# Kernel tuning notes

Measured on AMD Instinct MI355X. Metric: run time of the kernel, lower is better.

The kernel has to match this reference:

```python
import jax, jax.numpy as jnp
import numpy as np

B, T, D, H = 256, 512, 512, 512


def setup_inputs() -> dict:
    key = jax.random.key(0)
    k0, k1, k2, k3 = jax.random.split(key, 4)
    sD = 1.0 / np.sqrt(D).astype(np.float32)
    sH = 1.0 / np.sqrt(H).astype(np.float32)
    return {
        "x": jax.random.normal(k0, (B, T, D), jnp.float32),
        "Wx": jax.random.normal(k1, (D, 4 * H), jnp.float32) * sD,
        "Wh": jax.random.normal(k2, (H, 4 * H), jnp.float32) * sH,
        "b": jnp.zeros((4 * H,), jnp.float32),
        "Wfc": jax.random.normal(k3, (H, 1), jnp.float32) * sH,
        "bfc": jnp.zeros((1,), jnp.float32),
    }


def reference(x, Wx, Wh, b, Wfc, bfc):
    # x: [B, T, D]. Flax LSTMCell gates (i, f, g, o):
    #   i,f,o = sigmoid(.), g = tanh(.); c' = f*c + i*g; h' = o*tanh(c')
    Bv, Tv, _ = x.shape
    Hv = Wh.shape[0]
    # Precompute all input projections in one big GEMM (same math, batched).
    xg = jnp.einsum('btd,dg->btg', x, Wx) + b  # [B, T, 4H]

    def step(carry, xt):
        c, h = carry
        gates = xt + h @ Wh                     # [B, 4H]
        i, f, g, o = jnp.split(gates, 4, axis=-1)
        c_new = jax.nn.sigmoid(f) * c + jax.nn.sigmoid(i) * jnp.tanh(g)
        h_new = jax.nn.sigmoid(o) * jnp.tanh(c_new)
        return (c_new, h_new), None

    c0 = jnp.zeros((Bv, Hv), x.dtype)
    h0 = jnp.zeros((Bv, Hv), x.dtype)
    (c_fin, h_fin), _ = jax.lax.scan(step, (c0, h0), jnp.swapaxes(xg, 0, 1))
    # fc applied to last timestep output (== final hidden state)
    return h_fin @ Wfc + bfc  # [B, 1]
```

## Files before the change

kernel.cpp:

```cpp
#include <hip/hip_runtime.h>
#include <hip/hip_bf16.h>


typedef _Float16 half8 __attribute__((ext_vector_type(8)));
typedef _Float16 half4 __attribute__((ext_vector_type(4)));
typedef int int4v __attribute__((ext_vector_type(4)));
typedef float float4v __attribute__((ext_vector_type(4)));

__device__ __forceinline__ void gl_lds16(const void* g, void* l) {
  __builtin_amdgcn_global_load_lds(
      (const __attribute__((address_space(1))) unsigned int*)g,
      (__attribute__((address_space(3))) unsigned int*)l, 16, 0, 0);
}

__device__ __forceinline__ float sigm(float v) { return 1.f / (1.f + __expf(-v)); }
__device__ __forceinline__ float tanh_(float v) { return 1.f - 2.f / (__expf(2.f * v) + 1.f); }

__global__ __launch_bounds__(256) void k_prep(
    const float* __restrict__ x, const float* __restrict__ Wx,
    const float* __restrict__ Wh, const float* __restrict__ b,
    _Float16* __restrict__ xf, _Float16* __restrict__ wxt,
    _Float16* __restrict__ wht, float* __restrict__ bp)
{
  const long NX8 = 67108864L / 8;
  const long NW  = 2048L * 512;
  const long TOT = NX8 + 2 * NW + 2048;
  long stride = (long)gridDim.x * blockDim.x;
  for (long id = (long)blockIdx.x * blockDim.x + threadIdx.x; id < TOT; id += stride) {
    if (id < NX8) {
      const float4v* p = (const float4v*)x + id * 2;
      float4v a = p[0], c = p[1];
      half8 o;
      o[0]=(_Float16)a[0]; o[1]=(_Float16)a[1]; o[2]=(_Float16)a[2]; o[3]=(_Float16)a[3];
      o[4]=(_Float16)c[0]; o[5]=(_Float16)c[1]; o[6]=(_Float16)c[2]; o[7]=(_Float16)c[3];
      ((half8*)xf)[id] = o;
    } else if (id < NX8 + NW) {
      long e = id - NX8;
      int np = (int)(e >> 9), k = (int)(e & 511);
      int j = np >> 2, gt = np & 3;
      wxt[e] = (_Float16)Wx[(long)k * 2048 + gt * 512 + j];
    } else if (id < NX8 + 2 * NW) {
      long e = id - NX8 - NW;
      int np = (int)(e >> 9), k = (int)(e & 511);
      int j = np >> 2, gt = np & 3;
      wht[e] = (_Float16)Wh[(long)k * 2048 + gt * 512 + j];
    } else {
      int np = (int)(id - NX8 - 2 * NW);
      int j = np >> 2, gt = np & 3;
      bp[np] = b[gt * 512 + j];
    }
  }
}

__global__ __launch_bounds__(256, 2) void k_gemm_xg(
    const _Float16* __restrict__ xf, const _Float16* __restrict__ wxt,
    const float* __restrict__ bp, _Float16* __restrict__ xg)
{
  __shared__ _Float16 As[128 * 32];
  __shared__ _Float16 Bs[128 * 32];
  const int tid = threadIdx.x;
  const int w = tid >> 6, l = tid & 63;
  const int mt = blockIdx.x >> 4, nt = blockIdx.x & 15;
  const int qr = (w >> 1) * 64, qc = (w & 1) * 64;
  float4v acc[4][4];
  #pragma unroll
  for (int i = 0; i < 4; ++i)
    #pragma unroll
    for (int j = 0; j < 4; ++j) acc[i][j] = (float4v){0.f, 0.f, 0.f, 0.f};
  const int lr = l >> 2, lc = (l & 3) * 8;
  for (int kt = 0; kt < 16; ++kt) {
    __syncthreads();
    #pragma unroll
    for (int i = 0; i < 2; ++i) {
      int chunk = i * 4 + w;
      gl_lds16(xf + ((long)(mt * 128 + chunk * 16 + lr)) * 512 + kt * 32 + lc, As + chunk * 512);
      gl_lds16(wxt + ((long)(nt * 128 + chunk * 16 + lr)) * 512 + kt * 32 + lc, Bs + chunk * 512);
    }
    __syncthreads();
    half8 af[4], bf[4];
    #pragma unroll
    for (int mi = 0; mi < 4; ++mi)
      af[mi] = *(const half8*)(As + (qr + mi * 16 + (l & 15)) * 32 + (l >> 4) * 8);
    #pragma unroll
    for (int ni = 0; ni < 4; ++ni)
      bf[ni] = *(const half8*)(Bs + (qc + ni * 16 + (l & 15)) * 32 + (l >> 4) * 8);
    #pragma unroll
    for (int mi = 0; mi < 4; ++mi)
      #pragma unroll
      for (int ni = 0; ni < 4; ++ni)
        acc[mi][ni] = __builtin_amdgcn_mfma_f32_16x16x32_f16(af[mi], bf[ni], acc[mi][ni], 0, 0, 0);
  }
  #pragma unroll
  for (int ni = 0; ni < 4; ++ni) {
    int col = nt * 128 + qc + ni * 16 + (l & 15);
    float bias = bp[col];
    #pragma unroll
    for (int mi = 0; mi < 4; ++mi) {
      long R0 = (long)mt * 128 + qr + mi * 16 + (l >> 4) * 4;
      #pragma unroll
      for (int r = 0; r < 4; ++r)
        xg[(R0 + r) * 2048 + col] = (_Float16)(acc[mi][ni][r] + bias);
    }
  }
}

__global__ __launch_bounds__(256, 1) void k_scan(
    const _Float16* __restrict__ xg, const _Float16* __restrict__ wht,
    const float* __restrict__ wfc, const float* __restrict__ bfc,
    _Float16* __restrict__ hsl, unsigned int* __restrict__ flags,
    float* __restrict__ out)
{
  __shared__ unsigned int wctr;
  const int tid = threadIdx.x;
  if (tid == 0) wctr = 0;
  __syncthreads();

  const int w = tid >> 6, l = tid & 63;
  const int q = l >> 4;
  const int m = l & 15;
  const int bb = blockIdx.x;
  const int slot = bb >> 3;
  const int g = (bb & 7) * 2 + (slot >> 4);
  const int s = slot & 15;

  int4v bw0[16], bw1[16];
  {
    const _Float16* b0 = wht + ((long)(s * 128 + (2 * w + 0) * 16 + m)) * 512 + q * 8;
    const _Float16* b1 = wht + ((long)(s * 128 + (2 * w + 1) * 16 + m)) * 512 + q * 8;
    #pragma unroll
    for (int kk = 0; kk < 16; ++kk) {
      bw0[kk] = *(const int4v*)(b0 + kk * 32);
      bw1[kk] = *(const int4v*)(b1 + kk * 32);
    }
    #pragma unroll
    for (int kk = 0; kk < 16; ++kk)
      asm volatile("" : "+v"(bw0[kk]), "+v"(bw1[kk]));
  }

  float c0 = 0.f, c1 = 0.f;
  const int j0 = s * 32 + 8 * w + q;
  const int j1 = s * 32 + 8 * w + 4 + q;
  const float wf0 = wfc[j0], wf1 = wfc[j1];
  unsigned int* fl = flags + g * 256;
  const _Float16* xgr = xg + ((long)(g * 16 + m)) * 512 * 2048 + s * 128 + q * 4;
  const _Float16* hrg = hsl + (long)g * 8192 + q * 128 + m * 8;
  _Float16* hw = hsl + (long)(g * 16 + s) * 512 + w * 128 + m * 8;

  half4 xc0 = *(const half4*)(xgr + (2 * w + 0) * 16);
  half4 xc1 = *(const half4*)(xgr + (2 * w + 1) * 16);

  for (int t = 0; t < 512; ++t) {
    const int pr = t & 1;
    const long tn = (t < 511) ? (long)(t + 1) : 511L;
    const half4 xn0 = *(const half4*)(xgr + tn * 2048 + (2 * w + 0) * 16);
    const half4 xn1 = *(const half4*)(xgr + tn * 2048 + (2 * w + 1) * 16);
    if (t) {
      if (w == 0 && l < 16 && l != s) {
        unsigned int* p = fl + l * 16;
        while (__hip_atomic_load(p, __ATOMIC_RELAXED, __HIP_MEMORY_SCOPE_AGENT)
               < (unsigned)t) {}
      }
      asm volatile("" ::: "memory");
      __syncthreads();
    }
    const _Float16* hr = hrg + pr * 131072;
    int4v av[16];
    #pragma unroll
    for (int kk = 0; kk < 16; ++kk)
      asm volatile("global_load_dwordx4 %0, %1, off sc0 sc1"
                   : "=&v"(av[kk]) : "v"(hr + kk * 512) : "memory");
    asm volatile("s_waitcnt vmcnt(0)" ::: "memory");
    __builtin_amdgcn_sched_barrier(0);

    float4v a0 = (float4v){0.f,0.f,0.f,0.f}, a1 = a0, b0v = a0, b1v = a0;
    #pragma unroll
    for (int kk = 0; kk < 8; ++kk) {
      a0 = __builtin_amdgcn_mfma_f32_16x16x32_f16(__builtin_bit_cast(half8, bw0[kk]),
                                                  __builtin_bit_cast(half8, av[kk]), a0, 0, 0, 0);
      a1 = __builtin_amdgcn_mfma_f32_16x16x32_f16(__builtin_bit_cast(half8, bw1[kk]),
                                                  __builtin_bit_cast(half8, av[kk]), a1, 0, 0, 0);
    }
    #pragma unroll
    for (int kk = 8; kk < 16; ++kk) {
      b0v = __builtin_amdgcn_mfma_f32_16x16x32_f16(__builtin_bit_cast(half8, bw0[kk]),
                                                   __builtin_bit_cast(half8, av[kk]), b0v, 0, 0, 0);
      b1v = __builtin_amdgcn_mfma_f32_16x16x32_f16(__builtin_bit_cast(half8, bw1[kk]),
                                                   __builtin_bit_cast(half8, av[kk]), b1v, 0, 0, 0);
    }
    a0 += b0v; a1 += b1v;
    float i0 = sigm(a0[0] + (float)xc0[0]);
    float f0 = sigm(a0[1] + (float)xc0[1]);
    float g0 = tanh_(a0[2] + (float)xc0[2]);
    float o0 = sigm(a0[3] + (float)xc0[3]);
    c0 = f0 * c0 + i0 * g0;
    float h0v = o0 * tanh_(c0);
    float i1 = sigm(a1[0] + (float)xc1[0]);
    float f1 = sigm(a1[1] + (float)xc1[1]);
    float g1 = tanh_(a1[2] + (float)xc1[2]);
    float o1 = sigm(a1[3] + (float)xc1[3]);
    c1 = f1 * c1 + i1 * g1;
    float h1v = o1 * tanh_(c1);
    unsigned int hb0 = (unsigned int)__builtin_bit_cast(unsigned short, (_Float16)h0v);
    unsigned int hb1 = (unsigned int)__builtin_bit_cast(unsigned short, (_Float16)h1v);
    unsigned int pb0 = __shfl_xor(hb0, 16);
    unsigned int pb1 = __shfl_xor(hb1, 16);
    unsigned int pair0 = hb0 | (pb0 << 16);
    unsigned int pair1 = hb1 | (pb1 << 16);
    unsigned int x0 = __shfl_xor(pair0, 32);
    unsigned int x1 = __shfl_xor(pair1, 32);
    if (q == 0) {
      int4v pk = {(int)pair0, (int)x0, (int)pair1, (int)x1};
      _Float16* dst = hw + (pr ^ 1) * 131072;
      asm volatile("global_store_dwordx4 %0, %1, off sc0 sc1"
                   :: "v"(dst), "v"(pk) : "memory");
    }
    if (t == 511) {
      float part = h0v * wf0 + h1v * wf1;
      part += __shfl_xor(part, 16);
      part += __shfl_xor(part, 32);
      if (l < 16) {
        float v = part;
        if (s == 0 && w == 0) v += bfc[0];
        atomicAdd(out + g * 16 + l, v);
      }
    } else {
      asm volatile("s_waitcnt vmcnt(0)" ::: "memory");
      if (l == 0) {
        unsigned int old = atomicAdd(&wctr, 1u);
        if (old == 4u * (unsigned)t + 3u)
          __hip_atomic_store(fl + s * 16, (unsigned)(t + 1),
                             __ATOMIC_RELAXED, __HIP_MEMORY_SCOPE_AGENT);
      }
    }
    xc0 = xn0; xc1 = xn1;
  }
}

extern "C" void kernel_launch(void* const* d_in, const int* in_sizes, int n_in,
                              void* d_out, int out_size, void* d_ws, size_t ws_size,
                              hipStream_t stream)
{
  const float* x   = (const float*)d_in[0];
  const float* Wx  = (const float*)d_in[1];
  const float* Wh  = (const float*)d_in[2];
  const float* b   = (const float*)d_in[3];
  const float* Wfc = (const float*)d_in[4];
  const float* bfc = (const float*)d_in[5];
  char* ws = (char*)d_ws;

  const size_t OFF_XG  = 0;
  const size_t OFF_XB  = 536870912UL;
  const size_t OFF_WXT = OFF_XB + 134217728UL;
  const size_t OFF_WHT = OFF_WXT + 2097152UL;
  const size_t OFF_BP  = OFF_WHT + 2097152UL;
  const size_t OFF_H   = OFF_BP + 8192UL;
  const size_t OFF_FL  = OFF_H + 524288UL;
  const size_t NEED    = OFF_FL + 16384UL;
  if (ws_size < NEED) return;

  _Float16* xgp = (_Float16*)(ws + OFF_XG);
  _Float16* xfp = (_Float16*)(ws + OFF_XB);
  _Float16* wxt = (_Float16*)(ws + OFF_WXT);
  _Float16* wht = (_Float16*)(ws + OFF_WHT);
  float*    bp  = (float*)(ws + OFF_BP);
  _Float16* hsl = (_Float16*)(ws + OFF_H);
  unsigned int* flg = (unsigned int*)(ws + OFF_FL);
  float* outp = (float*)d_out;

  hipMemsetAsync(ws + OFF_H, 0, 262144, stream);
  hipMemsetAsync(ws + OFF_FL, 0, 16384, stream);
  hipMemsetAsync(d_out, 0, sizeof(float) * 256, stream);

  k_prep<<<4096, 256, 0, stream>>>(x, Wx, Wh, b, xfp, wxt, wht, bp);
  k_gemm_xg<<<16384, 256, 0, stream>>>(xfp, wxt, bp, xgp);

  const _Float16* xgc = xgp;
  const _Float16* whtc = wht;
  void* args[] = { (void*)&xgc, (void*)&whtc, (void*)&Wfc, (void*)&bfc,
                   (void*)&hsl, (void*)&flg, (void*)&outp };
  hipLaunchCooperativeKernel((void*)k_scan, dim3(256), dim3(256), args, 0, stream);
}
```

Before: 1.854 ms.

## Replace flag-based step sync with poisoned ring buffer of hidden states

Removes the per-step flag counters, LDS atomic and block barrier, and instead detects readiness of peer hidden-state slices by polling the data itself. A four-slot ring buffer is used and the slot two steps ahead is pre-filled with an all-ones poison pattern; readers reload until no poison words remain. This aims to cut synchronisation latency on the serial timestep chain, at the cost of redundant reloads while spinning and reliance on the poison pattern never appearing in real data and on store ordering across workgroups.

```diff
diff --git a/kernel.cpp b/kernel.cpp
--- a/kernel.cpp
+++ b/kernel.cpp
@@ -107,14 +107,9 @@
 __global__ __launch_bounds__(256, 1) void k_scan(
     const _Float16* __restrict__ xg, const _Float16* __restrict__ wht,
     const float* __restrict__ wfc, const float* __restrict__ bfc,
-    _Float16* __restrict__ hsl, unsigned int* __restrict__ flags,
-    float* __restrict__ out)
-{
-  __shared__ unsigned int wctr;
+    _Float16* __restrict__ hsl, float* __restrict__ out)
+{
   const int tid = threadIdx.x;
-  if (tid == 0) wctr = 0;
-  __syncthreads();
-
   const int w = tid >> 6, l = tid & 63;
   const int q = l >> 4;
   const int m = l & 15;
@@ -141,36 +136,48 @@
   const int j0 = s * 32 + 8 * w + q;
   const int j1 = s * 32 + 8 * w + 4 + q;
   const float wf0 = wfc[j0], wf1 = wfc[j1];
-  unsigned int* fl = flags + g * 256;
   const _Float16* xgr = xg + ((long)(g * 16 + m)) * 512 * 2048 + s * 128 + q * 4;
   const _Float16* hrg = hsl + (long)g * 8192 + q * 128 + m * 8;
   _Float16* hw = hsl + (long)(g * 16 + s) * 512 + w * 128 + m * 8;
+  const int4v POIS = {-1, -1, -1, -1};
 
   half4 xc0 = *(const half4*)(xgr + (2 * w + 0) * 16);
   half4 xc1 = *(const half4*)(xgr + (2 * w + 1) * 16);
 
   for (int t = 0; t < 512; ++t) {
-    const int pr = t & 1;
     const long tn = (t < 511) ? (long)(t + 1) : 511L;
     const half4 xn0 = *(const half4*)(xgr + tn * 2048 + (2 * w + 0) * 16);
     const half4 xn1 = *(const half4*)(xgr + tn * 2048 + (2 * w + 1) * 16);
-    if (t) {
-      if (w == 0 && l < 16 && l != s) {
-        unsigned int* p = fl + l * 16;
-        while (__hip_atomic_load(p, __ATOMIC_RELAXED, __HIP_MEMORY_SCOPE_AGENT)
-               < (unsigned)t) {}
+
+    if (q == 0) {
+      _Float16* pz = hw + (long)((t + 2) & 3) * 131072;
+      asm volatile("global_store_dwordx4 %0, %1, off sc0 sc1"
+                   :: "v"(pz), "v"(POIS) : "memory");
+    }
+
+    const _Float16* hr = hrg + (long)(t & 3) * 131072;
+    int4v av[16];
+    for (int spin = 0; ; ++spin) {
+      #pragma unroll
+      for (int kq = 0; kq < 4; ++kq) {
+        asm volatile(
+            "global_load_dwordx4 %0, %4, off sc0 sc1\n\t"
+            "global_load_dwordx4 %1, %4, off offset:1024 sc0 sc1\n\t"
+            "global_load_dwordx4 %2, %4, off offset:2048 sc0 sc1\n\t"
+            "global_load_dwordx4 %3, %4, off offset:3072 sc0 sc1"
+            : "=&v"(av[kq * 4 + 0]), "=&v"(av[kq * 4 + 1]),
+              "=&v"(av[kq * 4 + 2]), "=&v"(av[kq * 4 + 3])
+            : "v"(hr + kq * 2048)
+            : "memory");
       }
-      asm volatile("" ::: "memory");
-      __syncthreads();
-    }
-    const _Float16* hr = hrg + pr * 131072;
-    int4v av[16];
-    #pragma unroll
-    for (int kk = 0; kk < 16; ++kk)
-      asm volatile("global_load_dwordx4 %0, %1, off sc0 sc1"
-                   : "=&v"(av[kk]) : "v"(hr + kk * 512) : "memory");
-    asm volatile("s_waitcnt vmcnt(0)" ::: "memory");
-    __builtin_amdgcn_sched_barrier(0);
+      asm volatile("s_waitcnt vmcnt(0)" ::: "memory");
+      __builtin_amdgcn_sched_barrier(0);
+      int ok = 1;
+      #pragma unroll
+      for (int kk = 0; kk < 16; ++kk)
+        ok &= (av[kk][0] != -1) & (av[kk][1] != -1) & (av[kk][2] != -1) & (av[kk][3] != -1);
+      if (__all(ok) || spin > (1 << 20)) break;
+    }
 
     float4v a0 = (float4v){0.f,0.f,0.f,0.f}, a1 = a0, b0v = a0, b1v = a0;
     #pragma unroll
@@ -208,12 +215,6 @@
     unsigned int pair1 = hb1 | (pb1 << 16);
     unsigned int x0 = __shfl_xor(pair0, 32);
     unsigned int x1 = __shfl_xor(pair1, 32);
-    if (q == 0) {
-      int4v pk = {(int)pair0, (int)x0, (int)pair1, (int)x1};
-      _Float16* dst = hw + (pr ^ 1) * 131072;
-      asm volatile("global_store_dwordx4 %0, %1, off sc0 sc1"
-                   :: "v"(dst), "v"(pk) : "memory");
-    }
     if (t == 511) {
       float part = h0v * wf0 + h1v * wf1;
       part += __shfl_xor(part, 16);
@@ -223,14 +224,11 @@
         if (s == 0 && w == 0) v += bfc[0];
         atomicAdd(out + g * 16 + l, v);
       }
-    } else {
-      asm volatile("s_waitcnt vmcnt(0)" ::: "memory");
-      if (l == 0) {
-        unsigned int old = atomicAdd(&wctr, 1u);
-        if (old == 4u * (unsigned)t + 3u)
-          __hip_atomic_store(fl + s * 16, (unsigned)(t + 1),
-                             __ATOMIC_RELAXED, __HIP_MEMORY_SCOPE_AGENT);
-      }
+    } else if (q == 0) {
+      int4v pk = {(int)pair0, (int)x0, (int)pair1, (int)x1};
+      _Float16* dst = hw + (long)((t + 1) & 3) * 131072;
+      asm volatile("global_store_dwordx4 %0, %1, off sc0 sc1"
+                   :: "v"(dst), "v"(pk) : "memory");
     }
     xc0 = xn0; xc1 = xn1;
   }
@@ -254,8 +252,7 @@
   const size_t OFF_WHT = OFF_WXT + 2097152UL;
   const size_t OFF_BP  = OFF_WHT + 2097152UL;
   const size_t OFF_H   = OFF_BP + 8192UL;
-  const size_t OFF_FL  = OFF_H + 524288UL;
-  const size_t NEED    = OFF_FL + 16384UL;
+  const size_t NEED    = OFF_H + 1048576UL;
   if (ws_size < NEED) return;
 
   _Float16* xgp = (_Float16*)(ws + OFF_XG);
@@ -264,11 +261,10 @@
   _Float16* wht = (_Float16*)(ws + OFF_WHT);
   float*    bp  = (float*)(ws + OFF_BP);
   _Float16* hsl = (_Float16*)(ws + OFF_H);
-  unsigned int* flg = (unsigned int*)(ws + OFF_FL);
   float* outp = (float*)d_out;
 
   hipMemsetAsync(ws + OFF_H, 0, 262144, stream);
-  hipMemsetAsync(ws + OFF_FL, 0, 16384, stream);
+  hipMemsetAsync(ws + OFF_H + 262144, 0xFF, 786432, stream);
   hipMemsetAsync(d_out, 0, sizeof(float) * 256, stream);
 
   k_prep<<<4096, 256, 0, stream>>>(x, Wx, Wh, b, xfp, wxt, wht, bp);
@@ -277,6 +273,6 @@
   const _Float16* xgc = xgp;
   const _Float16* whtc = wht;
   void* args[] = { (void*)&xgc, (void*)&whtc, (void*)&Wfc, (void*)&bfc,
-                   (void*)&hsl, (void*)&flg, (void*)&outp };
+                   (void*)&hsl, (void*)&outp };
   hipLaunchCooperativeKernel((void*)k_scan, dim3(256), dim3(256), args, 0, stream);
 }
```

Result: slower. 2.420 ms (+30.5%).
